# Kernel optimization log

Measured on AMD Instinct MI355X. Metric: run time of the kernel, lower is better.

Reference implementation:

```python
import jax, jax.numpy as jnp
import numpy as np


def setup_inputs() -> dict:
    key = jax.random.key(0)
    k1, k2 = jax.random.split(key)
    imgs = jax.random.normal(k1, (4, 16, 64, 64), dtype=jnp.float32)
    kernel = jax.random.normal(k2, (16, 16, 5, 5), dtype=jnp.float32)
    return {"imgs": imgs, "kernel": kernel, "stride": 1, "padding": 2}


def reference(imgs, kernel, stride, padding):
    # Tropical-max (T+) semifield convolution (morphological dilation):
    #   multiply = add, add_reduce = max, zero = -inf, kind='conv' (kernel flipped)
    B, C, H, W = imgs.shape
    O, _, kH, kW = kernel.shape
    x = jnp.pad(imgs, ((0, 0), (0, 0), (padding, padding), (padding, padding)),
                constant_values=-jnp.inf)
    # kind='conv' flips the kernel spatially
    k = kernel[:, :, ::-1, ::-1]
    # im2col-style window extraction: [B, C*kH*kW, oH, oW], channel-major (C, kH, kW)
    patches = jax.lax.conv_general_dilated_patches(
        x, (kH, kW), (stride, stride), padding="VALID")
    oH, oW = patches.shape[2], patches.shape[3]
    win = patches.reshape(B, 1, C, kH, kW, oH, oW)
    w = k.reshape(1, O, C, kH, kW, 1, 1)
    # broadcast semifield multiply (add), then semifield reduce (max) over (C, kH, kW)
    out = jnp.max(win + w, axis=(2, 3, 4))  # [B, O, oH, oW]
    return out
```

## Files before the change

### kernel.cpp

```cpp
#include <hip/hip_runtime.h>
#include <math.h>


#define NEG_INF (-__builtin_inff())

__global__ __launch_bounds__(256, 4) void bconv_kernel(
        const float* __restrict__ img,
        const float* __restrict__ kern,
        float* __restrict__ out) {
    const int x  = threadIdx.x & 63;
    const int w  = threadIdx.x >> 6;
    const int y  = blockIdx.x;
    const int og = blockIdx.y;
    const int b  = blockIdx.z;
    const int o0 = og * 4;
    const int c0 = w * 4;

    __shared__ float red[4][4][64];

    int  xc[5];
    bool xok[5];
#pragma unroll
    for (int j = 0; j < 5; ++j) {
        int xx = x + j - 2;
        xok[j] = (unsigned)xx < 64u;
        xc[j]  = xok[j] ? xx : 0;
    }

    float acc0 = NEG_INF, acc1 = NEG_INF, acc2 = NEG_INF, acc3 = NEG_INF;

#pragma unroll
    for (int cc = 0; cc < 4; ++cc) {
        const int c = c0 + cc;
        const float* __restrict__ ic = img + ((b * 16 + c) << 12);
        const float* __restrict__ k0 = kern + ((o0 + 0) * 16 + c) * 25;
        const float* __restrict__ k1 = kern + ((o0 + 1) * 16 + c) * 25;
        const float* __restrict__ k2 = kern + ((o0 + 2) * 16 + c) * 25;
        const float* __restrict__ k3 = kern + ((o0 + 3) * 16 + c) * 25;
#pragma unroll
        for (int i = 0; i < 5; ++i) {
            const int yy = y + i - 2;
            if ((unsigned)yy >= 64u) continue;
            const float* __restrict__ rp = ic + (yy << 6);
            float v[5];
#pragma unroll
            for (int j = 0; j < 5; ++j) {
                float t = rp[xc[j]];
                v[j] = xok[j] ? t : NEG_INF;
            }
            const int kb = (4 - i) * 5 + 4;
#define ACC_O(kp, A)                                            \
            {                                                   \
                float t0 = v[0] + kp[kb - 0];                   \
                float t1 = v[1] + kp[kb - 1];                   \
                float t2 = v[2] + kp[kb - 2];                   \
                float t3 = v[3] + kp[kb - 3];                   \
                float t4 = v[4] + kp[kb - 4];                   \
                A = fmaxf(A, fmaxf(t0, t1));                    \
                A = fmaxf(A, fmaxf(t2, t3));                    \
                A = fmaxf(A, t4);                               \
            }
            ACC_O(k0, acc0)
            ACC_O(k1, acc1)
            ACC_O(k2, acc2)
            ACC_O(k3, acc3)
#undef ACC_O
        }
    }

    red[w][0][x] = acc0;
    red[w][1][x] = acc1;
    red[w][2][x] = acc2;
    red[w][3][x] = acc3;
    __syncthreads();

    const int oo = threadIdx.x >> 6;
    float r = fmaxf(fmaxf(red[0][oo][x], red[1][oo][x]),
                    fmaxf(red[2][oo][x], red[3][oo][x]));
    out[(((b * 16 + o0 + oo) << 6) + y) * 64 + x] = r;
}

extern "C" void kernel_launch(void* const* d_in, const int* in_sizes, int n_in,
                              void* d_out, int out_size, void* d_ws, size_t ws_size,
                              hipStream_t stream) {
    const float* img  = (const float*)d_in[0];
    const float* kern = (const float*)d_in[1];
    float* out = (float*)d_out;
    (void)in_sizes; (void)n_in; (void)out_size; (void)d_ws; (void)ws_size;

    dim3 grid(64, 4, 4);
    dim3 block(256);
    hipLaunchKernelGGL(bconv_kernel, grid, block, 0, stream, img, kern, out);
}
```

Baseline: 76.27 us.

## Pre-pad input with -inf in a separate kernel to remove bounds checks

Adds a pad kernel that writes a -inf bordered 68x68 copy of each input plane into workspace, so the dilation kernel loads a full 5x5 window without per-element bounds checks or per-row branches. The warp index is made wave-uniform with readfirstlane so weight loads can become scalar. This trades an extra kernel launch and an extra pass over the input through global memory for simpler, branch-free inner loops. It also relies on the workspace being large enough to hold the padded input.

After: 66.40 us. -12.9%, faster.

```diff
diff --git a/kernel.cpp b/kernel.cpp
--- a/kernel.cpp
+++ b/kernel.cpp
@@ -4,12 +4,29 @@
 
 #define NEG_INF (-__builtin_inff())
 
+#define PW 68
+#define PPLANE (PW * PW)
+
+__global__ __launch_bounds__(256) void pad_kernel(
+        const float* __restrict__ img, float* __restrict__ pad) {
+    const int idx   = blockIdx.x * 256 + threadIdx.x;
+    const int plane = idx / PPLANE;
+    const int rem   = idx % PPLANE;
+    const int py    = rem / PW;
+    const int px    = rem % PW;
+    const int yy = py - 2, xx = px - 2;
+    float v = NEG_INF;
+    if ((unsigned)yy < 64u && (unsigned)xx < 64u)
+        v = img[(plane << 12) + (yy << 6) + xx];
+    pad[idx] = v;
+}
+
 __global__ __launch_bounds__(256, 4) void bconv_kernel(
-        const float* __restrict__ img,
+        const float* __restrict__ pad,
         const float* __restrict__ kern,
         float* __restrict__ out) {
     const int x  = threadIdx.x & 63;
-    const int w  = threadIdx.x >> 6;
+    const int w  = __builtin_amdgcn_readfirstlane(threadIdx.x >> 6);
     const int y  = blockIdx.x;
     const int og = blockIdx.y;
     const int b  = blockIdx.z;
@@ -18,54 +35,43 @@
 
     __shared__ float red[4][4][64];
 
-    int  xc[5];
-    bool xok[5];
-#pragma unroll
-    for (int j = 0; j < 5; ++j) {
-        int xx = x + j - 2;
-        xok[j] = (unsigned)xx < 64u;
-        xc[j]  = xok[j] ? xx : 0;
-    }
-
     float acc0 = NEG_INF, acc1 = NEG_INF, acc2 = NEG_INF, acc3 = NEG_INF;
 
 #pragma unroll
     for (int cc = 0; cc < 4; ++cc) {
         const int c = c0 + cc;
-        const float* __restrict__ ic = img + ((b * 16 + c) << 12);
-        const float* __restrict__ k0 = kern + ((o0 + 0) * 16 + c) * 25;
-        const float* __restrict__ k1 = kern + ((o0 + 1) * 16 + c) * 25;
-        const float* __restrict__ k2 = kern + ((o0 + 2) * 16 + c) * 25;
-        const float* __restrict__ k3 = kern + ((o0 + 3) * 16 + c) * 25;
+        const float* __restrict__ pl = pad + (b * 16 + c) * PPLANE + y * PW + x;
+
+        float v[25];
 #pragma unroll
-        for (int i = 0; i < 5; ++i) {
-            const int yy = y + i - 2;
-            if ((unsigned)yy >= 64u) continue;
-            const float* __restrict__ rp = ic + (yy << 6);
-            float v[5];
+        for (int i = 0; i < 5; ++i)
 #pragma unroll
-            for (int j = 0; j < 5; ++j) {
-                float t = rp[xc[j]];
-                v[j] = xok[j] ? t : NEG_INF;
-            }
-            const int kb = (4 - i) * 5 + 4;
-#define ACC_O(kp, A)                                            \
-            {                                                   \
-                float t0 = v[0] + kp[kb - 0];                   \
-                float t1 = v[1] + kp[kb - 1];                   \
-                float t2 = v[2] + kp[kb - 2];                   \
-                float t3 = v[3] + kp[kb - 3];                   \
-                float t4 = v[4] + kp[kb - 4];                   \
-                A = fmaxf(A, fmaxf(t0, t1));                    \
-                A = fmaxf(A, fmaxf(t2, t3));                    \
-                A = fmaxf(A, t4);                               \
-            }
-            ACC_O(k0, acc0)
-            ACC_O(k1, acc1)
-            ACC_O(k2, acc2)
-            ACC_O(k3, acc3)
+            for (int j = 0; j < 5; ++j)
+                v[i * 5 + j] = pl[i * PW + j];
+
+#define ACC_O(oo, A)                                                     \
+        {                                                                \
+            const float* __restrict__ kp = kern + ((o0 + oo) * 16 + c) * 25; \
+            float kw[25];                                                \
+            _Pragma("unroll")                                            \
+            for (int t = 0; t < 25; ++t) kw[t] = kp[t];                  \
+            _Pragma("unroll")                                            \
+            for (int g = 0; g < 5; ++g) {                                \
+                float t0 = v[g * 5 + 0] + kw[24 - (g * 5 + 0)];          \
+                float t1 = v[g * 5 + 1] + kw[24 - (g * 5 + 1)];          \
+                float t2 = v[g * 5 + 2] + kw[24 - (g * 5 + 2)];          \
+                float t3 = v[g * 5 + 3] + kw[24 - (g * 5 + 3)];          \
+                float t4 = v[g * 5 + 4] + kw[24 - (g * 5 + 4)];          \
+                A = fmaxf(A, fmaxf(t0, t1));                             \
+                A = fmaxf(A, fmaxf(t2, t3));                             \
+                A = fmaxf(A, t4);                                        \
+            }                                                            \
+        }
+        ACC_O(0, acc0)
+        ACC_O(1, acc1)
+        ACC_O(2, acc2)
+        ACC_O(3, acc3)
 #undef ACC_O
-        }
     }
 
     red[w][0][x] = acc0;
@@ -86,9 +92,11 @@
     const float* img  = (const float*)d_in[0];
     const float* kern = (const float*)d_in[1];
     float* out = (float*)d_out;
-    (void)in_sizes; (void)n_in; (void)out_size; (void)d_ws; (void)ws_size;
+    float* pad = (float*)d_ws;
+    (void)in_sizes; (void)n_in; (void)out_size; (void)ws_size;
+
+    hipLaunchKernelGGL(pad_kernel, dim3(1156), dim3(256), 0, stream, img, pad);
 
     dim3 grid(64, 4, 4);
-    dim3 block(256);
-    hipLaunchKernelGGL(bconv_kernel, grid, block, 0, stream, img, kern, out);
+    hipLaunchKernelGGL(bconv_kernel, grid, dim3(256), 0, stream, pad, kern, out);
 }
```

## Split channels across eight waves and share row pixels via lane shuffles

Applied to the files above, without the earlier changes.

Doubles the block to 512 threads so each wave handles 2 input channels instead of 4, giving more waves per output tile to hide latency. The five overlapping horizontal loads per row become one load plus four cross-lane shuffles, and the wave index is made uniform with readfirstlane so kernel weights can use scalar loads. The channel loop is no longer unrolled, and the final reduction now combines eight partial maxima per output. Costs include the shuffle instructions, a larger shared reduction buffer, and half the threads sitting idle during the final write.

Measured after the change: 65.74 us. -13.8%, faster.

```diff
diff --git a/kernel.cpp b/kernel.cpp
--- a/kernel.cpp
+++ b/kernel.cpp
@@ -4,66 +4,66 @@
 
 #define NEG_INF (-__builtin_inff())
 
-__global__ __launch_bounds__(256, 4) void bconv_kernel(
+__global__ __launch_bounds__(512, 8) void bconv_kernel(
         const float* __restrict__ img,
         const float* __restrict__ kern,
         float* __restrict__ out) {
     const int x  = threadIdx.x & 63;
-    const int w  = threadIdx.x >> 6;
+    const int w  = __builtin_amdgcn_readfirstlane(threadIdx.x >> 6);
     const int y  = blockIdx.x;
     const int og = blockIdx.y;
     const int b  = blockIdx.z;
     const int o0 = og * 4;
-    const int c0 = w * 4;
+    const int c0 = w * 2;
 
-    __shared__ float red[4][4][64];
+    __shared__ float red[8][4][64];
 
-    int  xc[5];
-    bool xok[5];
-#pragma unroll
-    for (int j = 0; j < 5; ++j) {
-        int xx = x + j - 2;
-        xok[j] = (unsigned)xx < 64u;
-        xc[j]  = xok[j] ? xx : 0;
-    }
+    const bool ok0 = (x >= 2);
+    const bool ok1 = (x >= 1);
+    const bool ok3 = (x <= 62);
+    const bool ok4 = (x <= 61);
 
     float acc0 = NEG_INF, acc1 = NEG_INF, acc2 = NEG_INF, acc3 = NEG_INF;
 
-#pragma unroll
-    for (int cc = 0; cc < 4; ++cc) {
+#pragma unroll 1
+    for (int cc = 0; cc < 2; ++cc) {
         const int c = c0 + cc;
-        const float* __restrict__ ic = img + ((b * 16 + c) << 12);
-        const float* __restrict__ k0 = kern + ((o0 + 0) * 16 + c) * 25;
-        const float* __restrict__ k1 = kern + ((o0 + 1) * 16 + c) * 25;
-        const float* __restrict__ k2 = kern + ((o0 + 2) * 16 + c) * 25;
-        const float* __restrict__ k3 = kern + ((o0 + 3) * 16 + c) * 25;
+        const float* __restrict__ pl = img + ((b * 16 + c) << 12);
+        const float* __restrict__ kp0 = kern + ((o0 + 0) * 16 + c) * 25;
+        const float* __restrict__ kp1 = kern + ((o0 + 1) * 16 + c) * 25;
+        const float* __restrict__ kp2 = kern + ((o0 + 2) * 16 + c) * 25;
+        const float* __restrict__ kp3 = kern + ((o0 + 3) * 16 + c) * 25;
+
 #pragma unroll
         for (int i = 0; i < 5; ++i) {
             const int yy = y + i - 2;
             if ((unsigned)yy >= 64u) continue;
-            const float* __restrict__ rp = ic + (yy << 6);
-            float v[5];
-#pragma unroll
-            for (int j = 0; j < 5; ++j) {
-                float t = rp[xc[j]];
-                v[j] = xok[j] ? t : NEG_INF;
+            float v2 = pl[(yy << 6) + x];
+            float v0 = __shfl(v2, x - 2);
+            float v1 = __shfl(v2, x - 1);
+            float v3 = __shfl(v2, x + 1);
+            float v4 = __shfl(v2, x + 2);
+            v0 = ok0 ? v0 : NEG_INF;
+            v1 = ok1 ? v1 : NEG_INF;
+            v3 = ok3 ? v3 : NEG_INF;
+            v4 = ok4 ? v4 : NEG_INF;
+
+            const int kb = 24 - 5 * i;
+#define ACC_O(kp, A)                                                     \
+            {                                                            \
+                float t0 = v0 + kp[kb - 0];                              \
+                float t1 = v1 + kp[kb - 1];                              \
+                float t2 = v2 + kp[kb - 2];                              \
+                float t3 = v3 + kp[kb - 3];                              \
+                float t4 = v4 + kp[kb - 4];                              \
+                float m01  = fmaxf(t0, t1);                              \
+                float m234 = fmaxf(fmaxf(t2, t3), t4);                   \
+                A = fmaxf(A, fmaxf(m01, m234));                          \
             }
-            const int kb = (4 - i) * 5 + 4;
-#define ACC_O(kp, A)                                            \
-            {                                                   \
-                float t0 = v[0] + kp[kb - 0];                   \
-                float t1 = v[1] + kp[kb - 1];                   \
-                float t2 = v[2] + kp[kb - 2];                   \
-                float t3 = v[3] + kp[kb - 3];                   \
-                float t4 = v[4] + kp[kb - 4];                   \
-                A = fmaxf(A, fmaxf(t0, t1));                    \
-                A = fmaxf(A, fmaxf(t2, t3));                    \
-                A = fmaxf(A, t4);                               \
-            }
-            ACC_O(k0, acc0)
-            ACC_O(k1, acc1)
-            ACC_O(k2, acc2)
-            ACC_O(k3, acc3)
+            ACC_O(kp0, acc0)
+            ACC_O(kp1, acc1)
+            ACC_O(kp2, acc2)
+            ACC_O(kp3, acc3)
 #undef ACC_O
         }
     }
@@ -74,10 +74,13 @@
     red[w][3][x] = acc3;
     __syncthreads();
 
-    const int oo = threadIdx.x >> 6;
-    float r = fmaxf(fmaxf(red[0][oo][x], red[1][oo][x]),
-                    fmaxf(red[2][oo][x], red[3][oo][x]));
-    out[(((b * 16 + o0 + oo) << 6) + y) * 64 + x] = r;
+    if (threadIdx.x < 256) {
+        const int oo = threadIdx.x >> 6;
+        float r = red[0][oo][x];
+#pragma unroll
+        for (int ww = 1; ww < 8; ++ww) r = fmaxf(r, red[ww][oo][x]);
+        out[((b * 16 + o0 + oo) << 12) + (y << 6) + x] = r;
+    }
 }
 
 extern "C" void kernel_launch(void* const* d_in, const int* in_sizes, int n_in,
@@ -89,6 +92,5 @@
     (void)in_sizes; (void)n_in; (void)out_size; (void)d_ws; (void)ws_size;
 
     dim3 grid(64, 4, 4);
-    dim3 block(256);
-    hipLaunchKernelGGL(bconv_kernel, grid, block, 0, stream, img, kern, out);
+    hipLaunchKernelGGL(bconv_kernel, grid, dim3(512), 0, stream, img, kern, out);
 }
```
